# Kernel tuning notes

Hardware: AMD Instinct MI355X
Metric: run time of the kernel (lower is better)

## Reference

```python
import jax, jax.numpy as jnp
import numpy as np

NUM_NODES = 80000
NUM_EDGES = 1280000
NUM_GRAPHS = 512
IN_DIM = 64
HID = 64
NUM_CLASSES = 10


def setup_inputs() -> dict:
    key = jax.random.key(0)
    ks = jax.random.split(key, 16)
    x = jax.random.normal(ks[0], (NUM_NODES, IN_DIM), dtype=jnp.float32)
    edge_index = jax.random.randint(ks[1], (2, NUM_EDGES), 0, NUM_NODES, dtype=jnp.int64)
    batch = jnp.sort(jax.random.randint(ks[2], (NUM_NODES,), 0, NUM_GRAPHS, dtype=jnp.int64))

    def glorot(k, shape):
        fan_in, fan_out = shape[1], shape[0]
        lim = jnp.sqrt(6.0 / (fan_in + fan_out))
        return jax.random.uniform(k, shape, dtype=jnp.float32, minval=-lim, maxval=lim)

    inp = {
        "x": x,
        "edge_index": edge_index,
        "batch": batch,
        # GraphConv layer 1: lin_rel (with bias) applied to aggregated neighbors, lin_root (no bias)
        "w_rel1": glorot(ks[3], (HID, IN_DIM)),
        "b_rel1": jnp.zeros((HID,), dtype=jnp.float32),
        "w_root1": glorot(ks[4], (HID, IN_DIM)),
        # layer 2
        "w_rel2": glorot(ks[5], (HID, HID)),
        "b_rel2": jnp.zeros((HID,), dtype=jnp.float32),
        "w_root2": glorot(ks[6], (HID, HID)),
        # layer 3
        "w_rel3": glorot(ks[7], (HID, HID)),
        "b_rel3": jnp.zeros((HID,), dtype=jnp.float32),
        "w_root3": glorot(ks[8], (HID, HID)),
        # final linear head
        "w_lin": glorot(ks[9], (NUM_CLASSES, HID)),
        "b_lin": jnp.zeros((NUM_CLASSES,), dtype=jnp.float32),
    }
    return inp


def _graph_conv(x, src, dst, w_rel, b_rel, w_root):
    # PyG GraphConv with aggr='add': out_i = W_rel @ (sum_{j in N(i)} x_j) + b_rel + W_root @ x_i
    agg = jax.ops.segment_sum(x[src], dst, num_segments=NUM_NODES)  # [N, d_in]
    return agg @ w_rel.T + b_rel + x @ w_root.T


def reference(x, edge_index, batch,
              w_rel1, b_rel1, w_root1,
              w_rel2, b_rel2, w_root2,
              w_rel3, b_rel3, w_root3,
              w_lin, b_lin):
    src, dst = edge_index[0], edge_index[1]
    h = jax.nn.relu(_graph_conv(x, src, dst, w_rel1, b_rel1, w_root1))
    h = jax.nn.relu(_graph_conv(h, src, dst, w_rel2, b_rel2, w_root2))
    h = _graph_conv(h, src, dst, w_rel3, b_rel3, w_root3)
    # global_mean_pool over graph ids
    sums = jax.ops.segment_sum(h, batch, num_segments=NUM_GRAPHS)          # [G, HID]
    counts = jax.ops.segment_sum(jnp.ones((h.shape[0],), h.dtype), batch, num_segments=NUM_GRAPHS)
    pooled = sums / jnp.maximum(counts, 1.0)[:, None]
    # dropout p=0.5 is identity at inference (training=False)
    return pooled @ w_lin.T + b_lin  # [G, NUM_CLASSES]
```

## Files before the change

### kernel.cpp

```cpp
#include <hip/hip_runtime.h>

#define N_NODES  80000
#define N_EDGES  1280000
#define N_GRAPHS 512
#define DIM      64
#define NCLS     10

#define ETILE    8192
#define NTILE    157
#define NCB      157
#define CBPAD    160

typedef short short8f __attribute__((ext_vector_type(8)));
typedef float float4f __attribute__((ext_vector_type(4)));

static __device__ __forceinline__ unsigned short f2bf(float f) {
    unsigned u = __float_as_uint(f);
    unsigned r = (u + 0x7FFFu + ((u >> 16) & 1u)) >> 16;
    return (unsigned short)r;
}
static __device__ __forceinline__ float bf_lo(unsigned v) { return __uint_as_float(v << 16); }
static __device__ __forceinline__ float bf_hi(unsigned v) { return __uint_as_float(v & 0xFFFF0000u); }

__global__ __launch_bounds__(256) void k_hist(const int* __restrict__ ei,
                                              int* __restrict__ hmat) {
    __shared__ int hist[NCB];
    int tile = blockIdx.x, t = threadIdx.x;
    for (int i = t; i < NCB; i += 256) hist[i] = 0;
    __syncthreads();
    int base = tile * ETILE;
    int end = base + ETILE; if (end > N_EDGES) end = N_EDGES;
    for (int i = base + t; i < end; i += 256)
        atomicAdd(&hist[ei[N_EDGES + i] >> 9], 1);
    __syncthreads();
    for (int i = t; i < NCB; i += 256) hmat[tile * CBPAD + i] = hist[i];
}

__global__ __launch_bounds__(256) void k_scanT(const int* __restrict__ hmat,
        int* __restrict__ obase, int* __restrict__ btot) {
    __shared__ int sa[256], sb[256];
    int b = blockIdx.x, t = threadIdx.x;
    int v = (t < NTILE) ? hmat[t * CBPAD + b] : 0;
    sa[t] = v; __syncthreads();
    int* sp = sa; int* dp = sb;
    for (int off = 1; off < 256; off <<= 1) {
        dp[t] = sp[t] + ((t >= off) ? sp[t - off] : 0);
        __syncthreads();
        int* tmp = sp; sp = dp; dp = tmp;
    }
    int incl = sp[t];
    if (t < NTILE) obase[t * CBPAD + b] = incl - v;
    if (t == NTILE - 1) btot[b] = incl;
}

__global__ __launch_bounds__(256) void k_scanB(const int* __restrict__ btot,
        int* __restrict__ bucketbase, int* __restrict__ rowptr) {
    __shared__ int sa[256], sb[256];
    int t = threadIdx.x;
    int v = (t < NCB) ? btot[t] : 0;
    sa[t] = v; __syncthreads();
    int* sp = sa; int* dp = sb;
    for (int off = 1; off < 256; off <<= 1) {
        dp[t] = sp[t] + ((t >= off) ? sp[t - off] : 0);
        __syncthreads();
        int* tmp = sp; sp = dp; dp = tmp;
    }
    int incl = sp[t];
    if (t < NCB) bucketbase[t] = incl - v;
    if (t == 0) { bucketbase[NCB] = N_EDGES; rowptr[N_NODES] = N_EDGES; }
}

__global__ __launch_bounds__(256) void k_scatter(const int* __restrict__ ei,
        const int* __restrict__ obase, const int* __restrict__ bucketbase,
        int* __restrict__ ebuf) {
    __shared__ int cur[NCB];
    int tile = blockIdx.x, t = threadIdx.x;
    for (int i = t; i < NCB; i += 256)
        cur[i] = bucketbase[i] + obase[tile * CBPAD + i];
    __syncthreads();
    int base = tile * ETILE;
    int end = base + ETILE; if (end > N_EDGES) end = N_EDGES;
    for (int i = base + t; i < end; i += 256) {
        int s = ei[i], d = ei[N_EDGES + i];
        int p = atomicAdd(&cur[d >> 9], 1);
        ebuf[p] = s | ((d & 511) << 17);
    }
}

__global__ __launch_bounds__(256) void k_csr(const int* __restrict__ ebuf,
        const int* __restrict__ bucketbase, int* __restrict__ rowptr,
        int* __restrict__ col) {
    __shared__ int cnt[512];
    __shared__ int sa[512], sb[512];
    __shared__ int cur[512];
    int b = blockIdx.x, t = threadIdx.x;
    int s = bucketbase[b], e = bucketbase[b + 1];
    cnt[t] = 0; cnt[t + 256] = 0;
    __syncthreads();
    for (int i = s + t; i < e; i += 256) atomicAdd(&cnt[ebuf[i] >> 17], 1);
    __syncthreads();
    sa[t] = cnt[t]; sa[t + 256] = cnt[t + 256];
    __syncthreads();
    int* sp = sa; int* dp = sb;
    for (int off = 1; off < 512; off <<= 1) {
        int i1 = t + 256;
        int v0 = sp[t]  + ((t  >= off) ? sp[t  - off] : 0);
        int v1 = sp[i1] + ((i1 >= off) ? sp[i1 - off] : 0);
        __syncthreads();
        dp[t] = v0; dp[i1] = v1;
        __syncthreads();
        int* tmp = sp; sp = dp; dp = tmp;
    }
    int node0 = b * 512;
    int base0 = s + sp[t] - cnt[t];
    int base1 = s + sp[t + 256] - cnt[t + 256];
    cur[t] = base0; cur[t + 256] = base1;
    if (node0 + t < N_NODES)       rowptr[node0 + t] = base0;
    if (node0 + t + 256 < N_NODES) rowptr[node0 + t + 256] = base1;
    __syncthreads();
    for (int i = s + t; i < e; i += 256) {
        int pk = ebuf[i];
        int p = atomicAdd(&cur[pk >> 17], 1);
        col[p] = pk & 0x1FFFF;
    }
}

__global__ __launch_bounds__(256) void k_prep2(const float* __restrict__ x,
        const float* __restrict__ wr1, const float* __restrict__ wo1,
        const float* __restrict__ wr2, const float* __restrict__ wo2,
        unsigned short* __restrict__ xb, unsigned short* __restrict__ wf) {
    int bid = blockIdx.x, t = threadIdx.x;
    if (bid < 5000) {
        int i = bid * 256 + t;
        float4 v = ((const float4*)x)[i];
        ushort4 o;
        o.x = f2bf(v.x); o.y = f2bf(v.y); o.z = f2bf(v.z); o.w = f2bf(v.w);
        ((ushort4*)xb)[i] = o;
    } else {
        int idx = (bid - 5000) * 256 + t;
        int j = idx & 7, lane = (idx >> 3) & 63;
        int ks = (idx >> 9) & 3, nt = (idx >> 11) & 3, l = idx >> 13;
        int k = ks * 32 + ((lane >> 4) & 3) * 8 + j;
        int n = nt * 16 + (lane & 15);
        const float* wr = (l == 0) ? wr1 : wr2;
        const float* wo = (l == 0) ? wo1 : wo2;
        float val = (k < 64) ? wr[n * 64 + k] : wo[n * 64 + (k - 64)];
        wf[idx] = f2bf(val);
    }
}

__global__ __launch_bounds__(256) void k_gather4(const unsigned short* __restrict__ Xbf,
        const int* __restrict__ rowptr, const int* __restrict__ col,
        unsigned short* __restrict__ agg) {
    const uint4* Xq = (const uint4*)Xbf;
    int t = threadIdx.x, w = t >> 6, lane = t & 63;
    int e = lane >> 3, c = lane & 7;
    int node = blockIdx.x * 4 + w;
    int start = rowptr[node], end = rowptr[node + 1];
    float acc[8] = {0.f, 0.f, 0.f, 0.f, 0.f, 0.f, 0.f, 0.f};
    int base = start;
    for (; base + 16 <= end; base += 16) {
        int i0 = col[base + e];
        int i1 = col[base + 8 + e];
        uint4 v0 = Xq[(size_t)i0 * 8 + c];
        uint4 v1 = Xq[(size_t)i1 * 8 + c];
        acc[0] += bf_lo(v0.x) + bf_lo(v1.x); acc[1] += bf_hi(v0.x) + bf_hi(v1.x);
        acc[2] += bf_lo(v0.y) + bf_lo(v1.y); acc[3] += bf_hi(v0.y) + bf_hi(v1.y);
        acc[4] += bf_lo(v0.z) + bf_lo(v1.z); acc[5] += bf_hi(v0.z) + bf_hi(v1.z);
        acc[6] += bf_lo(v0.w) + bf_lo(v1.w); acc[7] += bf_hi(v0.w) + bf_hi(v1.w);
    }
    for (; base + 8 <= end; base += 8) {
        int i0 = col[base + e];
        uint4 v0 = Xq[(size_t)i0 * 8 + c];
        acc[0] += bf_lo(v0.x); acc[1] += bf_hi(v0.x);
        acc[2] += bf_lo(v0.y); acc[3] += bf_hi(v0.y);
        acc[4] += bf_lo(v0.z); acc[5] += bf_hi(v0.z);
        acc[6] += bf_lo(v0.w); acc[7] += bf_hi(v0.w);
    }
    int r = end - base;
    if (e < r) {
        int i0 = col[base + e];
        uint4 v0 = Xq[(size_t)i0 * 8 + c];
        acc[0] += bf_lo(v0.x); acc[1] += bf_hi(v0.x);
        acc[2] += bf_lo(v0.y); acc[3] += bf_hi(v0.y);
        acc[4] += bf_lo(v0.z); acc[5] += bf_hi(v0.z);
        acc[6] += bf_lo(v0.w); acc[7] += bf_hi(v0.w);
    }
#pragma unroll
    for (int off = 8; off < 64; off <<= 1) {
#pragma unroll
        for (int j = 0; j < 8; ++j) acc[j] += __shfl_xor(acc[j], off);
    }
    if (e == 0) {
        uint4 o;
        o.x = (unsigned)f2bf(acc[0]) | ((unsigned)f2bf(acc[1]) << 16);
        o.y = (unsigned)f2bf(acc[2]) | ((unsigned)f2bf(acc[3]) << 16);
        o.z = (unsigned)f2bf(acc[4]) | ((unsigned)f2bf(acc[5]) << 16);
        o.w = (unsigned)f2bf(acc[6]) | ((unsigned)f2bf(acc[7]) << 16);
        ((uint4*)agg)[(size_t)node * 8 + c] = o;
    }
}

__global__ __launch_bounds__(256) void k_linear_mfma(
        const unsigned short* __restrict__ aggb, const unsigned short* __restrict__ xb,
        const unsigned short* __restrict__ wf, const float* __restrict__ bias,
        unsigned short* __restrict__ out, int relu) {
    int t = threadIdx.x, w = t >> 6, lane = t & 63;
    int quad = lane >> 4, l15 = lane & 15;
    int mbase = blockIdx.x * 64 + w * 16;
    size_t arow = (size_t)(mbase + l15) * 64;
    short8f a0 = *(const short8f*)(aggb + arow + quad * 8);
    short8f a1 = *(const short8f*)(aggb + arow + 32 + quad * 8);
    short8f a2 = *(const short8f*)(xb   + arow + quad * 8);
    short8f a3 = *(const short8f*)(xb   + arow + 32 + quad * 8);
    int orow = mbase + quad * 4;
#pragma unroll
    for (int nt = 0; nt < 4; ++nt) {
        const unsigned short* wp = wf + ((size_t)(nt * 4) * 64 + lane) * 8;
        short8f b0 = *(const short8f*)(wp);
        short8f b1 = *(const short8f*)(wp + 64 * 8);
        short8f b2 = *(const short8f*)(wp + 128 * 8);
        short8f b3 = *(const short8f*)(wp + 192 * 8);
        float4f acc = {0.f, 0.f, 0.f, 0.f};
        acc = __builtin_amdgcn_mfma_f32_16x16x32_bf16(a0, b0, acc, 0, 0, 0);
        acc = __builtin_amdgcn_mfma_f32_16x16x32_bf16(a1, b1, acc, 0, 0, 0);
        acc = __builtin_amdgcn_mfma_f32_16x16x32_bf16(a2, b2, acc, 0, 0, 0);
        acc = __builtin_amdgcn_mfma_f32_16x16x32_bf16(a3, b3, acc, 0, 0, 0);
        float bi = bias[nt * 16 + l15];
#pragma unroll
        for (int r = 0; r < 4; ++r) {
            float v = acc[r] + bi;
            if (relu) v = fmaxf(v, 0.f);
            out[(size_t)(orow + r) * 64 + nt * 16 + l15] = f2bf(v);
        }
    }
}

static __device__ __forceinline__ int lowerb(const int* a, int n, int key) {
    int lo = 0, hi = n;
    while (lo < hi) { int mid = (lo + hi) >> 1; if (a[mid] < key) lo = mid + 1; else hi = mid; }
    return lo;
}

__global__ __launch_bounds__(256) void k_gsum(const unsigned short* __restrict__ h2,
        const int* __restrict__ rowptr, const int* __restrict__ col,
        const int* __restrict__ batch, float* __restrict__ S4) {
    __shared__ float red1[8][64];
    __shared__ float red2[8][64];
    const unsigned* Xu = (const unsigned*)h2;
    int g = blockIdx.x >> 2, part = blockIdx.x & 3;
    int t = threadIdx.x;
    int hw = t >> 5, c = t & 31;
    int ns = lowerb(batch, N_NODES, g);
    int ne = lowerb(batch, N_NODES, g + 1);
    int a0 = ns + (int)(((long long)(ne - ns) * part) >> 2);
    int a1 = ns + (int)(((long long)(ne - ns) * (part + 1)) >> 2);
    int es = rowptr[a0], ee = rowptr[a1];
    float alo = 0.f, ahi = 0.f;
    int nfull = (ee - es) >> 7;
    int e0 = es + hw * 16;
    for (int b = 0; b < nfull; ++b, e0 += 128) {
        unsigned v[16];
#pragma unroll
        for (int j = 0; j < 16; ++j)
            v[j] = Xu[(size_t)col[e0 + j] * 32 + c];
#pragma unroll
        for (int j = 0; j < 16; ++j) { alo += bf_lo(v[j]); ahi += bf_hi(v[j]); }
    }
    for (int e = es + nfull * 128 + hw; e < ee; e += 8) {
        unsigned v = Xu[(size_t)col[e] * 32 + c];
        alo += bf_lo(v); ahi += bf_hi(v);
    }
    float blo = 0.f, bhi = 0.f;
    for (int i = a0 + hw; i < a1; i += 8) {
        unsigned v = Xu[(size_t)i * 32 + c];
        blo += bf_lo(v); bhi += bf_hi(v);
    }
    red1[hw][2 * c] = alo; red1[hw][2 * c + 1] = ahi;
    red2[hw][2 * c] = blo; red2[hw][2 * c + 1] = bhi;
    __syncthreads();
    if (t < 64) {
        float v = 0.f;
#pragma unroll
        for (int s = 0; s < 8; ++s) v += red1[s][t];
        S4[(size_t)blockIdx.x * 128 + t] = v;
    } else if (t < 128) {
        float v = 0.f;
#pragma unroll
        for (int s = 0; s < 8; ++s) v += red2[s][t - 64];
        S4[(size_t)blockIdx.x * 128 + 64 + (t - 64)] = v;
    }
}

__global__ __launch_bounds__(64) void k_head2(const float* __restrict__ S4,
        const int* __restrict__ batch,
        const float* __restrict__ wr3, const float* __restrict__ wo3,
        const float* __restrict__ b3,
        const float* __restrict__ wlin, const float* __restrict__ blin,
        float* __restrict__ out) {
    __shared__ float s1[64], s2[64], pl[64];
    int g = blockIdx.x, t = threadIdx.x;
    int ns = lowerb(batch, N_NODES, g);
    int ne = lowerb(batch, N_NODES, g + 1);
    float inv = 1.f / (float)((ne > ns) ? (ne - ns) : 1);
    const float* Sg = S4 + (size_t)g * 4 * 128;
    s1[t] = (Sg[t]       + Sg[128 + t]       + Sg[256 + t]       + Sg[384 + t]) * inv;
    s2[t] = (Sg[64 + t]  + Sg[192 + t]       + Sg[320 + t]       + Sg[448 + t]) * inv;
    __syncthreads();
    float acc = b3[t];
    for (int k = 0; k < 64; ++k)
        acc += s1[k] * wr3[t * 64 + k] + s2[k] * wo3[t * 64 + k];
    pl[t] = acc;
    __syncthreads();
    float myout = 0.f;
    for (int cls = 0; cls < NCLS; ++cls) {
        float vv = pl[t] * wlin[cls * 64 + t];
        for (int off = 32; off > 0; off >>= 1) vv += __shfl_xor(vv, off);
        if (t == cls) myout = vv + blin[cls];
    }
    if (t < NCLS) out[g * NCLS + t] = myout;
}

extern "C" void kernel_launch(void* const* d_in, const int* in_sizes, int n_in,
                              void* d_out, int out_size, void* d_ws, size_t ws_size,
                              hipStream_t stream) {
    const float* x     = (const float*)d_in[0];
    const int*   ei    = (const int*)d_in[1];
    const int*   batch = (const int*)d_in[2];
    const float* wr1 = (const float*)d_in[3];
    const float* b1  = (const float*)d_in[4];
    const float* wo1 = (const float*)d_in[5];
    const float* wr2 = (const float*)d_in[6];
    const float* b2  = (const float*)d_in[7];
    const float* wo2 = (const float*)d_in[8];
    const float* wr3 = (const float*)d_in[9];
    const float* b3  = (const float*)d_in[10];
    const float* wo3 = (const float*)d_in[11];
    const float* wlin = (const float*)d_in[12];
    const float* blin = (const float*)d_in[13];
    float* out = (float*)d_out;

    char* p = (char*)d_ws;
    auto alloc = [&](size_t bytes) { char* r = p; p += (bytes + 255) & ~(size_t)255; return r; };
    int*   rowptr  = (int*)alloc((N_NODES + 1) * sizeof(int));
    int*   hmat    = (int*)alloc((size_t)NTILE * CBPAD * sizeof(int));
    int*   obase   = (int*)alloc((size_t)NTILE * CBPAD * sizeof(int));
    int*   btot    = (int*)alloc(CBPAD * sizeof(int));
    int*   bucketbase = (int*)alloc((NCB + 1) * sizeof(int));
    int*   ebuf    = (int*)alloc((size_t)N_EDGES * sizeof(int));
    int*   col     = (int*)alloc((size_t)N_EDGES * sizeof(int));
    unsigned short* wf  = (unsigned short*)alloc(2 * 8192 * sizeof(unsigned short));
    unsigned short* xbf = (unsigned short*)alloc((size_t)N_NODES * 64 * 2);
    unsigned short* agg = (unsigned short*)alloc((size_t)N_NODES * 64 * 2);
    unsigned short* hA  = (unsigned short*)alloc((size_t)N_NODES * 64 * 2);
    unsigned short* hB  = (unsigned short*)alloc((size_t)N_NODES * 64 * 2);
    float* S4      = (float*)alloc((size_t)N_GRAPHS * 4 * 128 * sizeof(float));

    k_hist   <<<NTILE, 256, 0, stream>>>(ei, hmat);
    k_scanT  <<<NCB,   256, 0, stream>>>(hmat, obase, btot);
    k_scanB  <<<1,     256, 0, stream>>>(btot, bucketbase, rowptr);
    k_scatter<<<NTILE, 256, 0, stream>>>(ei, obase, bucketbase, ebuf);
    k_csr    <<<NCB,   256, 0, stream>>>(ebuf, bucketbase, rowptr, col);
    k_prep2  <<<5064,  256, 0, stream>>>(x, wr1, wo1, wr2, wo2, xbf, wf);

    k_gather4    <<<N_NODES / 4,  256, 0, stream>>>(xbf, rowptr, col, agg);
    k_linear_mfma<<<N_NODES / 64, 256, 0, stream>>>(agg, xbf, wf,        b1, hA, 1);
    k_gather4    <<<N_NODES / 4,  256, 0, stream>>>(hA, rowptr, col, agg);
    k_linear_mfma<<<N_NODES / 64, 256, 0, stream>>>(agg, hA, wf + 8192,  b2, hB, 1);
    k_gsum <<<N_GRAPHS * 4, 256, 0, stream>>>(hB, rowptr, col, batch, S4);
    k_head2<<<N_GRAPHS,     64,  0, stream>>>(S4, batch, wr3, wo3, b3, wlin, blin, out);
}
```

Baseline: 268.3 us.

## Split node features into column-chunk planes to shrink gather working set

Stores bf16 node features in four planes of 16 columns each, so each gather and pooling pass runs per chunk over a 2.5 MB table instead of one 10 MB table. The intent is better L2/cache hit rates for the random neighbor gathers. The MFMA linear kernel, pooling and head are rewritten to read and write the chunked layout, and the edge index loads use nontemporal hints. The cost is reading the CSR column indices four times per layer and using narrower 8-byte loads.

```diff
diff --git a/kernel.cpp b/kernel.cpp
--- a/kernel.cpp
+++ b/kernel.cpp
@@ -11,8 +11,13 @@
 #define NCB      157
 #define CBPAD    160
 
+#define NCHUNK   4
+#define CHW      16
+#define CHB      ((size_t)N_NODES * CHW)
+
 typedef short short8f __attribute__((ext_vector_type(8)));
 typedef float float4f __attribute__((ext_vector_type(4)));
+typedef unsigned uint2v __attribute__((ext_vector_type(2)));
 
 static __device__ __forceinline__ unsigned short f2bf(float f) {
     unsigned u = __float_as_uint(f);
@@ -132,10 +137,11 @@
     int bid = blockIdx.x, t = threadIdx.x;
     if (bid < 5000) {
         int i = bid * 256 + t;
+        int node = i >> 4, f4 = i & 15;
         float4 v = ((const float4*)x)[i];
         ushort4 o;
         o.x = f2bf(v.x); o.y = f2bf(v.y); o.z = f2bf(v.z); o.w = f2bf(v.w);
-        ((ushort4*)xb)[i] = o;
+        ((ushort4*)xb)[(size_t)(f4 >> 2) * (N_NODES * 4) + (size_t)node * 4 + (f4 & 3)] = o;
     } else {
         int idx = (bid - 5000) * 256 + t;
         int j = idx & 7, lane = (idx >> 3) & 63;
@@ -149,55 +155,50 @@
     }
 }
 
-__global__ __launch_bounds__(256) void k_gather4(const unsigned short* __restrict__ Xbf,
+__global__ __launch_bounds__(256) void k_gather_c(const unsigned short* __restrict__ Xc,
         const int* __restrict__ rowptr, const int* __restrict__ col,
-        unsigned short* __restrict__ agg) {
-    const uint4* Xq = (const uint4*)Xbf;
+        unsigned short* __restrict__ aggc) {
     int t = threadIdx.x, w = t >> 6, lane = t & 63;
-    int e = lane >> 3, c = lane & 7;
+    int e = lane >> 2, c = lane & 3;
+    int ch = blockIdx.y;
     int node = blockIdx.x * 4 + w;
+    const uint2v* Xq = (const uint2v*)(Xc + (size_t)ch * CHB);
     int start = rowptr[node], end = rowptr[node + 1];
-    float acc[8] = {0.f, 0.f, 0.f, 0.f, 0.f, 0.f, 0.f, 0.f};
+    float a0 = 0.f, a1 = 0.f, a2 = 0.f, a3 = 0.f;
     int base = start;
-    for (; base + 16 <= end; base += 16) {
-        int i0 = col[base + e];
-        int i1 = col[base + 8 + e];
-        uint4 v0 = Xq[(size_t)i0 * 8 + c];
-        uint4 v1 = Xq[(size_t)i1 * 8 + c];
-        acc[0] += bf_lo(v0.x) + bf_lo(v1.x); acc[1] += bf_hi(v0.x) + bf_hi(v1.x);
-        acc[2] += bf_lo(v0.y) + bf_lo(v1.y); acc[3] += bf_hi(v0.y) + bf_hi(v1.y);
-        acc[4] += bf_lo(v0.z) + bf_lo(v1.z); acc[5] += bf_hi(v0.z) + bf_hi(v1.z);
-        acc[6] += bf_lo(v0.w) + bf_lo(v1.w); acc[7] += bf_hi(v0.w) + bf_hi(v1.w);
-    }
-    for (; base + 8 <= end; base += 8) {
-        int i0 = col[base + e];
-        uint4 v0 = Xq[(size_t)i0 * 8 + c];
-        acc[0] += bf_lo(v0.x); acc[1] += bf_hi(v0.x);
-        acc[2] += bf_lo(v0.y); acc[3] += bf_hi(v0.y);
-        acc[4] += bf_lo(v0.z); acc[5] += bf_hi(v0.z);
-        acc[6] += bf_lo(v0.w); acc[7] += bf_hi(v0.w);
+    for (; base + 32 <= end; base += 32) {
+        int i0 = __builtin_nontemporal_load(col + base + e);
+        int i1 = __builtin_nontemporal_load(col + base + 16 + e);
+        uint2v v0 = Xq[(size_t)i0 * 4 + c];
+        uint2v v1 = Xq[(size_t)i1 * 4 + c];
+        a0 += bf_lo(v0.x) + bf_lo(v1.x); a1 += bf_hi(v0.x) + bf_hi(v1.x);
+        a2 += bf_lo(v0.y) + bf_lo(v1.y); a3 += bf_hi(v0.y) + bf_hi(v1.y);
+    }
+    if (base + 16 <= end) {
+        int i0 = __builtin_nontemporal_load(col + base + e);
+        uint2v v0 = Xq[(size_t)i0 * 4 + c];
+        a0 += bf_lo(v0.x); a1 += bf_hi(v0.x);
+        a2 += bf_lo(v0.y); a3 += bf_hi(v0.y);
+        base += 16;
     }
     int r = end - base;
     if (e < r) {
         int i0 = col[base + e];
-        uint4 v0 = Xq[(size_t)i0 * 8 + c];
-        acc[0] += bf_lo(v0.x); acc[1] += bf_hi(v0.x);
-        acc[2] += bf_lo(v0.y); acc[3] += bf_hi(v0.y);
-        acc[4] += bf_lo(v0.z); acc[5] += bf_hi(v0.z);
-        acc[6] += bf_lo(v0.w); acc[7] += bf_hi(v0.w);
-    }
-#pragma unroll
-    for (int off = 8; off < 64; off <<= 1) {
-#pragma unroll
-        for (int j = 0; j < 8; ++j) acc[j] += __shfl_xor(acc[j], off);
+        uint2v v0 = Xq[(size_t)i0 * 4 + c];
+        a0 += bf_lo(v0.x); a1 += bf_hi(v0.x);
+        a2 += bf_lo(v0.y); a3 += bf_hi(v0.y);
+    }
+#pragma unroll
+    for (int off = 4; off < 64; off <<= 1) {
+        a0 += __shfl_xor(a0, off); a1 += __shfl_xor(a1, off);
+        a2 += __shfl_xor(a2, off); a3 += __shfl_xor(a3, off);
     }
     if (e == 0) {
-        uint4 o;
-        o.x = (unsigned)f2bf(acc[0]) | ((unsigned)f2bf(acc[1]) << 16);
-        o.y = (unsigned)f2bf(acc[2]) | ((unsigned)f2bf(acc[3]) << 16);
-        o.z = (unsigned)f2bf(acc[4]) | ((unsigned)f2bf(acc[5]) << 16);
-        o.w = (unsigned)f2bf(acc[6]) | ((unsigned)f2bf(acc[7]) << 16);
-        ((uint4*)agg)[(size_t)node * 8 + c] = o;
+        uint2v o;
+        o.x = (unsigned)f2bf(a0) | ((unsigned)f2bf(a1) << 16);
+        o.y = (unsigned)f2bf(a2) | ((unsigned)f2bf(a3) << 16);
+        __builtin_nontemporal_store(o,
+            (uint2v*)(aggc + (size_t)ch * CHB) + (size_t)node * 4 + c);
     }
 }
 
@@ -208,11 +209,13 @@
     int t = threadIdx.x, w = t >> 6, lane = t & 63;
     int quad = lane >> 4, l15 = lane & 15;
     int mbase = blockIdx.x * 64 + w * 16;
-    size_t arow = (size_t)(mbase + l15) * 64;
-    short8f a0 = *(const short8f*)(aggb + arow + quad * 8);
-    short8f a1 = *(const short8f*)(aggb + arow + 32 + quad * 8);
-    short8f a2 = *(const short8f*)(xb   + arow + quad * 8);
-    short8f a3 = *(const short8f*)(xb   + arow + 32 + quad * 8);
+    int m = mbase + l15;
+    size_t roff = (size_t)m * CHW + (quad & 1) * 8;
+    int qh = quad >> 1;
+    short8f a0 = *(const short8f*)(aggb + (size_t)qh * CHB + roff);
+    short8f a1 = *(const short8f*)(aggb + (size_t)(2 + qh) * CHB + roff);
+    short8f a2 = *(const short8f*)(xb   + (size_t)qh * CHB + roff);
+    short8f a3 = *(const short8f*)(xb   + (size_t)(2 + qh) * CHB + roff);
     int orow = mbase + quad * 4;
 #pragma unroll
     for (int nt = 0; nt < 4; ++nt) {
@@ -231,7 +234,7 @@
         for (int r = 0; r < 4; ++r) {
             float v = acc[r] + bi;
             if (relu) v = fmaxf(v, 0.f);
-            out[(size_t)(orow + r) * 64 + nt * 16 + l15] = f2bf(v);
+            out[(size_t)nt * CHB + (size_t)(orow + r) * CHW + l15] = f2bf(v);
         }
     }
 }
@@ -242,15 +245,16 @@
     return lo;
 }
 
-__global__ __launch_bounds__(256) void k_gsum(const unsigned short* __restrict__ h2,
+__global__ __launch_bounds__(256) void k_gsum_c(const unsigned short* __restrict__ h2,
         const int* __restrict__ rowptr, const int* __restrict__ col,
         const int* __restrict__ batch, float* __restrict__ S4) {
-    __shared__ float red1[8][64];
-    __shared__ float red2[8][64];
-    const unsigned* Xu = (const unsigned*)h2;
+    __shared__ float red1[32][16];
+    __shared__ float red2[32][16];
+    int ch = blockIdx.y;
     int g = blockIdx.x >> 2, part = blockIdx.x & 3;
     int t = threadIdx.x;
-    int hw = t >> 5, c = t & 31;
+    int hw = t >> 3, c = t & 7;
+    const unsigned* Xu = (const unsigned*)(h2 + (size_t)ch * CHB);
     int ns = lowerb(batch, N_NODES, g);
     int ne = lowerb(batch, N_NODES, g + 1);
     int a0 = ns + (int)(((long long)(ne - ns) * part) >> 2);
@@ -258,37 +262,41 @@
     int es = rowptr[a0], ee = rowptr[a1];
     float alo = 0.f, ahi = 0.f;
     int nfull = (ee - es) >> 7;
-    int e0 = es + hw * 16;
+    int e0 = es + hw;
     for (int b = 0; b < nfull; ++b, e0 += 128) {
-        unsigned v[16];
-#pragma unroll
-        for (int j = 0; j < 16; ++j)
-            v[j] = Xu[(size_t)col[e0 + j] * 32 + c];
-#pragma unroll
-        for (int j = 0; j < 16; ++j) { alo += bf_lo(v[j]); ahi += bf_hi(v[j]); }
-    }
-    for (int e = es + nfull * 128 + hw; e < ee; e += 8) {
-        unsigned v = Xu[(size_t)col[e] * 32 + c];
+        int i0 = __builtin_nontemporal_load(col + e0);
+        int i1 = __builtin_nontemporal_load(col + e0 + 32);
+        int i2 = __builtin_nontemporal_load(col + e0 + 64);
+        int i3 = __builtin_nontemporal_load(col + e0 + 96);
+        unsigned v0 = Xu[(size_t)i0 * 8 + c];
+        unsigned v1 = Xu[(size_t)i1 * 8 + c];
+        unsigned v2 = Xu[(size_t)i2 * 8 + c];
+        unsigned v3 = Xu[(size_t)i3 * 8 + c];
+        alo += bf_lo(v0) + bf_lo(v1) + bf_lo(v2) + bf_lo(v3);
+        ahi += bf_hi(v0) + bf_hi(v1) + bf_hi(v2) + bf_hi(v3);
+    }
+    for (int e2 = es + nfull * 128 + hw; e2 < ee; e2 += 32) {
+        unsigned v = Xu[(size_t)col[e2] * 8 + c];
         alo += bf_lo(v); ahi += bf_hi(v);
     }
     float blo = 0.f, bhi = 0.f;
-    for (int i = a0 + hw; i < a1; i += 8) {
-        unsigned v = Xu[(size_t)i * 32 + c];
+    for (int i = a0 + hw; i < a1; i += 32) {
+        unsigned v = Xu[(size_t)i * 8 + c];
         blo += bf_lo(v); bhi += bf_hi(v);
     }
     red1[hw][2 * c] = alo; red1[hw][2 * c + 1] = ahi;
     red2[hw][2 * c] = blo; red2[hw][2 * c + 1] = bhi;
     __syncthreads();
-    if (t < 64) {
+    if (t < 16) {
         float v = 0.f;
 #pragma unroll
-        for (int s = 0; s < 8; ++s) v += red1[s][t];
-        S4[(size_t)blockIdx.x * 128 + t] = v;
-    } else if (t < 128) {
+        for (int s = 0; s < 32; ++s) v += red1[s][t];
+        S4[(((size_t)g * 4 + ch) * 4 + part) * 32 + t] = v;
+    } else if (t < 32) {
         float v = 0.f;
 #pragma unroll
-        for (int s = 0; s < 8; ++s) v += red2[s][t - 64];
-        S4[(size_t)blockIdx.x * 128 + 64 + (t - 64)] = v;
+        for (int s = 0; s < 32; ++s) v += red2[s][t - 16];
+        S4[(((size_t)g * 4 + ch) * 4 + part) * 32 + 16 + (t - 16)] = v;
     }
 }
 
@@ -303,13 +311,14 @@
     int ns = lowerb(batch, N_NODES, g);
     int ne = lowerb(batch, N_NODES, g + 1);
     float inv = 1.f / (float)((ne > ns) ? (ne - ns) : 1);
-    const float* Sg = S4 + (size_t)g * 4 * 128;
-    s1[t] = (Sg[t]       + Sg[128 + t]       + Sg[256 + t]       + Sg[384 + t]) * inv;
-    s2[t] = (Sg[64 + t]  + Sg[192 + t]       + Sg[320 + t]       + Sg[448 + t]) * inv;
+    int ch = t >> 4, k = t & 15;
+    const float* Sg = S4 + ((size_t)g * 4 + ch) * 128;
+    s1[t] = (Sg[k]      + Sg[32 + k] + Sg[64 + k] + Sg[96 + k])  * inv;
+    s2[t] = (Sg[16 + k] + Sg[48 + k] + Sg[80 + k] + Sg[112 + k]) * inv;
     __syncthreads();
     float acc = b3[t];
-    for (int k = 0; k < 64; ++k)
-        acc += s1[k] * wr3[t * 64 + k] + s2[k] * wo3[t * 64 + k];
+    for (int k2 = 0; k2 < 64; ++k2)
+        acc += s1[k2] * wr3[t * 64 + k2] + s2[k2] * wo3[t * 64 + k2];
     pl[t] = acc;
     __syncthreads();
     float myout = 0.f;
@@ -363,10 +372,10 @@
     k_csr    <<<NCB,   256, 0, stream>>>(ebuf, bucketbase, rowptr, col);
     k_prep2  <<<5064,  256, 0, stream>>>(x, wr1, wo1, wr2, wo2, xbf, wf);
 
-    k_gather4    <<<N_NODES / 4,  256, 0, stream>>>(xbf, rowptr, col, agg);
+    k_gather_c   <<<dim3(N_NODES / 4, NCHUNK), 256, 0, stream>>>(xbf, rowptr, col, agg);
     k_linear_mfma<<<N_NODES / 64, 256, 0, stream>>>(agg, xbf, wf,        b1, hA, 1);
-    k_gather4    <<<N_NODES / 4,  256, 0, stream>>>(hA, rowptr, col, agg);
+    k_gather_c   <<<dim3(N_NODES / 4, NCHUNK), 256, 0, stream>>>(hA, rowptr, col, agg);
     k_linear_mfma<<<N_NODES / 64, 256, 0, stream>>>(agg, hA, wf + 8192,  b2, hB, 1);
-    k_gsum <<<N_GRAPHS * 4, 256, 0, stream>>>(hB, rowptr, col, batch, S4);
-    k_head2<<<N_GRAPHS,     64,  0, stream>>>(S4, batch, wr3, wo3, b3, wlin, blin, out);
-}
+    k_gsum_c<<<dim3(N_GRAPHS * 4, NCHUNK), 256, 0, stream>>>(hB, rowptr, col, batch, S4);
+    k_head2 <<<N_GRAPHS, 64, 0, stream>>>(S4, batch, wr3, wo3, b3, wlin, blin, out);
+}
```

Result: slower. 413.5 us (+54.1%).

## Fuse neighbor gather with MFMA linear and merge CSR-build launches

Applied to the files above, without the earlier changes.

The gather and the MFMA linear layer become one kernel. Each wave aggregates 16 nodes into LDS and then feeds the MFMA directly, so the bf16 aggregate buffer is no longer written to and re-read from global memory. The edge histogram and the x/weight bf16 conversion are merged into one launch. The single-block bucket scan is dropped and recomputed redundantly inside the scatter and CSR kernels, which cuts the launch count. In exchange, each wave now processes 16 nodes one after another instead of one node per wave, which reduces memory-level parallelism in the latency-bound gather.

```diff
diff --git a/kernel.cpp b/kernel.cpp
--- a/kernel.cpp
+++ b/kernel.cpp
@@ -22,18 +22,44 @@
 static __device__ __forceinline__ float bf_lo(unsigned v) { return __uint_as_float(v << 16); }
 static __device__ __forceinline__ float bf_hi(unsigned v) { return __uint_as_float(v & 0xFFFF0000u); }
 
-__global__ __launch_bounds__(256) void k_hist(const int* __restrict__ ei,
-                                              int* __restrict__ hmat) {
+__global__ __launch_bounds__(256) void k_histprep(const int* __restrict__ ei,
+        const float* __restrict__ x,
+        const float* __restrict__ wr1, const float* __restrict__ wo1,
+        const float* __restrict__ wr2, const float* __restrict__ wo2,
+        int* __restrict__ hmat, unsigned short* __restrict__ xb,
+        unsigned short* __restrict__ wf) {
     __shared__ int hist[NCB];
-    int tile = blockIdx.x, t = threadIdx.x;
-    for (int i = t; i < NCB; i += 256) hist[i] = 0;
-    __syncthreads();
-    int base = tile * ETILE;
-    int end = base + ETILE; if (end > N_EDGES) end = N_EDGES;
-    for (int i = base + t; i < end; i += 256)
-        atomicAdd(&hist[ei[N_EDGES + i] >> 9], 1);
-    __syncthreads();
-    for (int i = t; i < NCB; i += 256) hmat[tile * CBPAD + i] = hist[i];
+    int bid = blockIdx.x, t = threadIdx.x;
+    if (bid < NTILE) {
+        int tile = bid;
+        for (int i = t; i < NCB; i += 256) hist[i] = 0;
+        __syncthreads();
+        int base = tile * ETILE;
+        int end = base + ETILE; if (end > N_EDGES) end = N_EDGES;
+        for (int i = base + t; i < end; i += 256)
+            atomicAdd(&hist[ei[N_EDGES + i] >> 9], 1);
+        __syncthreads();
+        for (int i = t; i < NCB; i += 256) hmat[tile * CBPAD + i] = hist[i];
+        return;
+    }
+    int pb = bid - NTILE;
+    if (pb < 5000) {
+        int i = pb * 256 + t;
+        float4 v = ((const float4*)x)[i];
+        ushort4 o;
+        o.x = f2bf(v.x); o.y = f2bf(v.y); o.z = f2bf(v.z); o.w = f2bf(v.w);
+        ((ushort4*)xb)[i] = o;
+    } else {
+        int idx = (pb - 5000) * 256 + t;
+        int j = idx & 7, lane = (idx >> 3) & 63;
+        int ks = (idx >> 9) & 3, nt = (idx >> 11) & 3, l = idx >> 13;
+        int k = ks * 32 + ((lane >> 4) & 3) * 8 + j;
+        int n = nt * 16 + (lane & 15);
+        const float* wr = (l == 0) ? wr1 : wr2;
+        const float* wo = (l == 0) ? wo1 : wo2;
+        float val = (k < 64) ? wr[n * 64 + k] : wo[n * 64 + (k - 64)];
+        wf[idx] = f2bf(val);
+    }
 }
 
 __global__ __launch_bounds__(256) void k_scanT(const int* __restrict__ hmat,
@@ -53,10 +79,12 @@
     if (t == NTILE - 1) btot[b] = incl;
 }
 
-__global__ __launch_bounds__(256) void k_scanB(const int* __restrict__ btot,
-        int* __restrict__ bucketbase, int* __restrict__ rowptr) {
+__global__ __launch_bounds__(256) void k_scatter2(const int* __restrict__ ei,
+        const int* __restrict__ obase, const int* __restrict__ btot,
+        int* __restrict__ ebuf) {
     __shared__ int sa[256], sb[256];
-    int t = threadIdx.x;
+    __shared__ int cur[NCB];
+    int tile = blockIdx.x, t = threadIdx.x;
     int v = (t < NCB) ? btot[t] : 0;
     sa[t] = v; __syncthreads();
     int* sp = sa; int* dp = sb;
@@ -65,18 +93,7 @@
         __syncthreads();
         int* tmp = sp; sp = dp; dp = tmp;
     }
-    int incl = sp[t];
-    if (t < NCB) bucketbase[t] = incl - v;
-    if (t == 0) { bucketbase[NCB] = N_EDGES; rowptr[N_NODES] = N_EDGES; }
-}
-
-__global__ __launch_bounds__(256) void k_scatter(const int* __restrict__ ei,
-        const int* __restrict__ obase, const int* __restrict__ bucketbase,
-        int* __restrict__ ebuf) {
-    __shared__ int cur[NCB];
-    int tile = blockIdx.x, t = threadIdx.x;
-    for (int i = t; i < NCB; i += 256)
-        cur[i] = bucketbase[i] + obase[tile * CBPAD + i];
+    if (t < NCB) cur[t] = (sp[t] - v) + obase[tile * CBPAD + t];
     __syncthreads();
     int base = tile * ETILE;
     int end = base + ETILE; if (end > N_EDGES) end = N_EDGES;
@@ -87,21 +104,32 @@
     }
 }
 
-__global__ __launch_bounds__(256) void k_csr(const int* __restrict__ ebuf,
-        const int* __restrict__ bucketbase, int* __restrict__ rowptr,
+__global__ __launch_bounds__(256) void k_csr2(const int* __restrict__ ebuf,
+        const int* __restrict__ btot, int* __restrict__ rowptr,
         int* __restrict__ col) {
     __shared__ int cnt[512];
     __shared__ int sa[512], sb[512];
     __shared__ int cur[512];
     int b = blockIdx.x, t = threadIdx.x;
-    int s = bucketbase[b], e = bucketbase[b + 1];
+    int v = (t < NCB) ? btot[t] : 0;
+    sa[t] = v; __syncthreads();
+    int* sp = sa; int* dp = sb;
+    for (int off = 1; off < 256; off <<= 1) {
+        dp[t] = sp[t] + ((t >= off) ? sp[t - off] : 0);
+        __syncthreads();
+        int* tmp = sp; sp = dp; dp = tmp;
+    }
+    int e = sp[b];
+    int s = e - btot[b];
+    if (b == 0 && t == 0) rowptr[N_NODES] = N_EDGES;
+    __syncthreads();
     cnt[t] = 0; cnt[t + 256] = 0;
     __syncthreads();
     for (int i = s + t; i < e; i += 256) atomicAdd(&cnt[ebuf[i] >> 17], 1);
     __syncthreads();
     sa[t] = cnt[t]; sa[t + 256] = cnt[t + 256];
     __syncthreads();
-    int* sp = sa; int* dp = sb;
+    sp = sa; dp = sb;
     for (int off = 1; off < 512; off <<= 1) {
         int i1 = t + 256;
         int v0 = sp[t]  + ((t  >= off) ? sp[t  - off] : 0);
@@ -125,95 +153,70 @@
     }
 }
 
-__global__ __launch_bounds__(256) void k_prep2(const float* __restrict__ x,
-        const float* __restrict__ wr1, const float* __restrict__ wo1,
-        const float* __restrict__ wr2, const float* __restrict__ wo2,
-        unsigned short* __restrict__ xb, unsigned short* __restrict__ wf) {
-    int bid = blockIdx.x, t = threadIdx.x;
-    if (bid < 5000) {
-        int i = bid * 256 + t;
-        float4 v = ((const float4*)x)[i];
-        ushort4 o;
-        o.x = f2bf(v.x); o.y = f2bf(v.y); o.z = f2bf(v.z); o.w = f2bf(v.w);
-        ((ushort4*)xb)[i] = o;
-    } else {
-        int idx = (bid - 5000) * 256 + t;
-        int j = idx & 7, lane = (idx >> 3) & 63;
-        int ks = (idx >> 9) & 3, nt = (idx >> 11) & 3, l = idx >> 13;
-        int k = ks * 32 + ((lane >> 4) & 3) * 8 + j;
-        int n = nt * 16 + (lane & 15);
-        const float* wr = (l == 0) ? wr1 : wr2;
-        const float* wo = (l == 0) ? wo1 : wo2;
-        float val = (k < 64) ? wr[n * 64 + k] : wo[n * 64 + (k - 64)];
-        wf[idx] = f2bf(val);
-    }
-}
-
-__global__ __launch_bounds__(256) void k_gather4(const unsigned short* __restrict__ Xbf,
+__global__ __launch_bounds__(256) void k_gatherlin(
+        const unsigned short* __restrict__ Xin,
         const int* __restrict__ rowptr, const int* __restrict__ col,
-        unsigned short* __restrict__ agg) {
-    const uint4* Xq = (const uint4*)Xbf;
+        const unsigned short* __restrict__ wf, const float* __restrict__ bias,
+        unsigned short* __restrict__ out, int relu) {
+    __shared__ uint4 sAgg[64][9];
+    const uint4* Xq = (const uint4*)Xin;
     int t = threadIdx.x, w = t >> 6, lane = t & 63;
     int e = lane >> 3, c = lane & 7;
-    int node = blockIdx.x * 4 + w;
-    int start = rowptr[node], end = rowptr[node + 1];
-    float acc[8] = {0.f, 0.f, 0.f, 0.f, 0.f, 0.f, 0.f, 0.f};
-    int base = start;
-    for (; base + 16 <= end; base += 16) {
-        int i0 = col[base + e];
-        int i1 = col[base + 8 + e];
-        uint4 v0 = Xq[(size_t)i0 * 8 + c];
-        uint4 v1 = Xq[(size_t)i1 * 8 + c];
-        acc[0] += bf_lo(v0.x) + bf_lo(v1.x); acc[1] += bf_hi(v0.x) + bf_hi(v1.x);
-        acc[2] += bf_lo(v0.y) + bf_lo(v1.y); acc[3] += bf_hi(v0.y) + bf_hi(v1.y);
-        acc[4] += bf_lo(v0.z) + bf_lo(v1.z); acc[5] += bf_hi(v0.z) + bf_hi(v1.z);
-        acc[6] += bf_lo(v0.w) + bf_lo(v1.w); acc[7] += bf_hi(v0.w) + bf_hi(v1.w);
-    }
-    for (; base + 8 <= end; base += 8) {
-        int i0 = col[base + e];
-        uint4 v0 = Xq[(size_t)i0 * 8 + c];
-        acc[0] += bf_lo(v0.x); acc[1] += bf_hi(v0.x);
-        acc[2] += bf_lo(v0.y); acc[3] += bf_hi(v0.y);
-        acc[4] += bf_lo(v0.z); acc[5] += bf_hi(v0.z);
-        acc[6] += bf_lo(v0.w); acc[7] += bf_hi(v0.w);
-    }
-    int r = end - base;
-    if (e < r) {
-        int i0 = col[base + e];
-        uint4 v0 = Xq[(size_t)i0 * 8 + c];
-        acc[0] += bf_lo(v0.x); acc[1] += bf_hi(v0.x);
-        acc[2] += bf_lo(v0.y); acc[3] += bf_hi(v0.y);
-        acc[4] += bf_lo(v0.z); acc[5] += bf_hi(v0.z);
-        acc[6] += bf_lo(v0.w); acc[7] += bf_hi(v0.w);
-    }
-#pragma unroll
-    for (int off = 8; off < 64; off <<= 1) {
-#pragma unroll
-        for (int j = 0; j < 8; ++j) acc[j] += __shfl_xor(acc[j], off);
-    }
-    if (e == 0) {
-        uint4 o;
-        o.x = (unsigned)f2bf(acc[0]) | ((unsigned)f2bf(acc[1]) << 16);
-        o.y = (unsigned)f2bf(acc[2]) | ((unsigned)f2bf(acc[3]) << 16);
-        o.z = (unsigned)f2bf(acc[4]) | ((unsigned)f2bf(acc[5]) << 16);
-        o.w = (unsigned)f2bf(acc[6]) | ((unsigned)f2bf(acc[7]) << 16);
-        ((uint4*)agg)[(size_t)node * 8 + c] = o;
-    }
-}
-
-__global__ __launch_bounds__(256) void k_linear_mfma(
-        const unsigned short* __restrict__ aggb, const unsigned short* __restrict__ xb,
-        const unsigned short* __restrict__ wf, const float* __restrict__ bias,
-        unsigned short* __restrict__ out, int relu) {
-    int t = threadIdx.x, w = t >> 6, lane = t & 63;
+    int nb = blockIdx.x * 64 + w * 16;
+    int rp = (lane <= 16) ? rowptr[nb + lane] : 0;
+    for (int n = 0; n < 16; ++n) {
+        int start = __shfl(rp, n), end = __shfl(rp, n + 1);
+        float acc[8] = {0.f, 0.f, 0.f, 0.f, 0.f, 0.f, 0.f, 0.f};
+        int base = start;
+        for (; base + 16 <= end; base += 16) {
+            int i0 = col[base + e];
+            int i1 = col[base + 8 + e];
+            uint4 v0 = Xq[(size_t)i0 * 8 + c];
+            uint4 v1 = Xq[(size_t)i1 * 8 + c];
+            acc[0] += bf_lo(v0.x) + bf_lo(v1.x); acc[1] += bf_hi(v0.x) + bf_hi(v1.x);
+            acc[2] += bf_lo(v0.y) + bf_lo(v1.y); acc[3] += bf_hi(v0.y) + bf_hi(v1.y);
+            acc[4] += bf_lo(v0.z) + bf_lo(v1.z); acc[5] += bf_hi(v0.z) + bf_hi(v1.z);
+            acc[6] += bf_lo(v0.w) + bf_lo(v1.w); acc[7] += bf_hi(v0.w) + bf_hi(v1.w);
+        }
+        for (; base + 8 <= end; base += 8) {
+            int i0 = col[base + e];
+            uint4 v0 = Xq[(size_t)i0 * 8 + c];
+            acc[0] += bf_lo(v0.x); acc[1] += bf_hi(v0.x);
+            acc[2] += bf_lo(v0.y); acc[3] += bf_hi(v0.y);
+            acc[4] += bf_lo(v0.z); acc[5] += bf_hi(v0.z);
+            acc[6] += bf_lo(v0.w); acc[7] += bf_hi(v0.w);
+        }
+        int r = end - base;
+        if (e < r) {
+            int i0 = col[base + e];
+            uint4 v0 = Xq[(size_t)i0 * 8 + c];
+            acc[0] += bf_lo(v0.x); acc[1] += bf_hi(v0.x);
+            acc[2] += bf_lo(v0.y); acc[3] += bf_hi(v0.y);
+            acc[4] += bf_lo(v0.z); acc[5] += bf_hi(v0.z);
+            acc[6] += bf_lo(v0.w); acc[7] += bf_hi(v0.w);
+        }
+#pragma unroll
+        for (int off = 8; off < 64; off <<= 1) {
+#pragma unroll
+            for (int j = 0; j < 8; ++j) acc[j] += __shfl_xor(acc[j], off);
+        }
+        if (e == 0) {
+            uint4 o;
+            o.x = (unsigned)f2bf(acc[0]) | ((unsigned)f2bf(acc[1]) << 16);
+            o.y = (unsigned)f2bf(acc[2]) | ((unsigned)f2bf(acc[3]) << 16);
+            o.z = (unsigned)f2bf(acc[4]) | ((unsigned)f2bf(acc[5]) << 16);
+            o.w = (unsigned)f2bf(acc[6]) | ((unsigned)f2bf(acc[7]) << 16);
+            sAgg[w * 16 + n][c] = o;
+        }
+    }
     int quad = lane >> 4, l15 = lane & 15;
-    int mbase = blockIdx.x * 64 + w * 16;
-    size_t arow = (size_t)(mbase + l15) * 64;
-    short8f a0 = *(const short8f*)(aggb + arow + quad * 8);
-    short8f a1 = *(const short8f*)(aggb + arow + 32 + quad * 8);
-    short8f a2 = *(const short8f*)(xb   + arow + quad * 8);
-    short8f a3 = *(const short8f*)(xb   + arow + 32 + quad * 8);
-    int orow = mbase + quad * 4;
+    int m = nb + l15;
+    short8f a0 = *(const short8f*)&sAgg[w * 16 + l15][quad];
+    short8f a1 = *(const short8f*)&sAgg[w * 16 + l15][4 + quad];
+    const unsigned short* xr = Xin + (size_t)m * 64;
+    short8f a2 = *(const short8f*)(xr + quad * 8);
+    short8f a3 = *(const short8f*)(xr + 32 + quad * 8);
+    int orow = nb + quad * 4;
 #pragma unroll
     for (int nt = 0; nt < 4; ++nt) {
         const unsigned short* wp = wf + ((size_t)(nt * 4) * 64 + lane) * 8;
@@ -346,27 +349,23 @@
     int*   hmat    = (int*)alloc((size_t)NTILE * CBPAD * sizeof(int));
     int*   obase   = (int*)alloc((size_t)NTILE * CBPAD * sizeof(int));
     int*   btot    = (int*)alloc(CBPAD * sizeof(int));
-    int*   bucketbase = (int*)alloc((NCB + 1) * sizeof(int));
     int*   ebuf    = (int*)alloc((size_t)N_EDGES * sizeof(int));
     int*   col     = (int*)alloc((size_t)N_EDGES * sizeof(int));
     unsigned short* wf  = (unsigned short*)alloc(2 * 8192 * sizeof(unsigned short));
     unsigned short* xbf = (unsigned short*)alloc((size_t)N_NODES * 64 * 2);
-    unsigned short* agg = (unsigned short*)alloc((size_t)N_NODES * 64 * 2);
     unsigned short* hA  = (unsigned short*)alloc((size_t)N_NODES * 64 * 2);
     unsigned short* hB  = (unsigned short*)alloc((size_t)N_NODES * 64 * 2);
     float* S4      = (float*)alloc((size_t)N_GRAPHS * 4 * 128 * sizeof(float));
 
-    k_hist   <<<NTILE, 256, 0, stream>>>(ei, hmat);
-    k_scanT  <<<NCB,   256, 0, stream>>>(hmat, obase, btot);
-    k_scanB  <<<1,     256, 0, stream>>>(btot, bucketbase, rowptr);
-    k_scatter<<<NTILE, 256, 0, stream>>>(ei, obase, bucketbase, ebuf);
-    k_csr    <<<NCB,   256, 0, stream>>>(ebuf, bucketbase, rowptr, col);
-    k_prep2  <<<5064,  256, 0, stream>>>(x, wr1, wo1, wr2, wo2, xbf, wf);
-
-    k_gather4    <<<N_NODES / 4,  256, 0, stream>>>(xbf, rowptr, col, agg);
-    k_linear_mfma<<<N_NODES / 64, 256, 0, stream>>>(agg, xbf, wf,        b1, hA, 1);
-    k_gather4    <<<N_NODES / 4,  256, 0, stream>>>(hA, rowptr, col, agg);
-    k_linear_mfma<<<N_NODES / 64, 256, 0, stream>>>(agg, hA, wf + 8192,  b2, hB, 1);
+    k_histprep<<<NTILE + 5064, 256, 0, stream>>>(ei, x, wr1, wo1, wr2, wo2,
+                                                 hmat, xbf, wf);
+    k_scanT   <<<NCB,   256, 0, stream>>>(hmat, obase, btot);
+    k_scatter2<<<NTILE, 256, 0, stream>>>(ei, obase, btot, ebuf);
+    k_csr2    <<<NCB,   256, 0, stream>>>(ebuf, btot, rowptr, col);
+
+    k_gatherlin<<<N_NODES / 64, 256, 0, stream>>>(xbf, rowptr, col, wf,        b1, hA, 1);
+    k_gatherlin<<<N_NODES / 64, 256, 0, stream>>>(hA,  rowptr, col, wf + 8192, b2, hB, 1);
+
     k_gsum <<<N_GRAPHS * 4, 256, 0, stream>>>(hB, rowptr, col, batch, S4);
     k_head2<<<N_GRAPHS,     64,  0, stream>>>(S4, batch, wr3, wo3, b3, wlin, blin, out);
 }
```

Result: faster. 261.7 us (-2.5%).
